# Optimization experiments

Measured on AMD Instinct MI355X. Metric: run time of the kernel, lower is better.

## Reference

```python
import jax, jax.numpy as jnp
import numpy as np

D_MODEL = 1024
H = 16
D_K = D_MODEL // H  # 64


def setup_inputs() -> dict:
    key = jax.random.key(0)
    ks = jax.random.split(key, 10)
    s = 1.0 / np.sqrt(D_MODEL)
    x = jax.random.normal(ks[0], (4, 2048, D_MODEL), dtype=jnp.float32)
    # Per-head linear weights stacked: [H, d_model, d_k]
    Wq = jax.random.uniform(ks[1], (H, D_MODEL, D_K), jnp.float32, -s, s)
    bq = jax.random.uniform(ks[2], (H, D_K), jnp.float32, -s, s)
    Wk = jax.random.uniform(ks[3], (H, D_MODEL, D_K), jnp.float32, -s, s)
    bk = jax.random.uniform(ks[4], (H, D_K), jnp.float32, -s, s)
    Wv = jax.random.uniform(ks[5], (H, D_MODEL, D_K), jnp.float32, -s, s)
    bv = jax.random.uniform(ks[6], (H, D_K), jnp.float32, -s, s)
    so = 1.0 / np.sqrt(H * D_K)
    Wo = jax.random.uniform(ks[7], (H * D_K, D_MODEL), jnp.float32, -so, so)
    bo = jax.random.uniform(ks[8], (D_MODEL,), jnp.float32, -so, so)
    return {"x": x, "Wq": Wq, "bq": bq, "Wk": Wk, "bk": bk, "Wv": Wv, "bv": bv, "Wo": Wo, "bo": bo}


def reference(x, Wq, bq, Wk, bk, Wv, bv, Wo, bo):
    # x: [B, S, D]; Wq/Wk/Wv: [H, D, d_k]; b*: [H, d_k]
    q = jnp.einsum('bsd,hdk->bhsk', x, Wq) + bq[None, :, None, :]
    k = jnp.einsum('bsd,hdk->bhsk', x, Wk) + bk[None, :, None, :]
    v = jnp.einsum('bsd,hdk->bhsk', x, Wv) + bv[None, :, None, :]
    scores = jnp.einsum('bhqk,bhsk->bhqs', q, k) / np.sqrt(D_K)
    S = x.shape[1]
    causal = jnp.triu(jnp.ones((S, S), dtype=bool), k=1)  # True above diagonal
    scores = jnp.where(causal, -jnp.inf, scores)
    attn = jax.nn.softmax(scores, axis=-1)
    ctx = jnp.einsum('bhqs,bhsk->bhqk', attn, v)  # [B, H, S, d_k]
    B = x.shape[0]
    # concat heads: torch cats head outputs along last dim -> [B, S, H*d_k]
    ctx = jnp.transpose(ctx, (0, 2, 1, 3)).reshape(B, S, H * D_K)
    return ctx @ Wo + bo
```

## Files before the change

kernel.cpp:

```cpp
#include <hip/hip_runtime.h>
#include <hip/hip_bf16.h>

typedef unsigned short u16;
typedef __attribute__((ext_vector_type(8))) short short8;
typedef __attribute__((ext_vector_type(4))) short short4v;
typedef __attribute__((ext_vector_type(4))) float floatx4;

#define D_MODEL 1024
#define NH 16
#define SEQ 2048
#define BATCH 4
#define M_ROWS 8192
#define N_QKV 3072
#define PS_LD 72

__device__ __forceinline__ u16 f2u(float f) {
    __hip_bfloat16 h = __float2bfloat16(f);
    u16 u; __builtin_memcpy(&u, &h, 2); return u;
}

__device__ __forceinline__ void async_copy16(const u16* g, u16* l) {
    __builtin_amdgcn_global_load_lds(
        (const __attribute__((address_space(1))) unsigned int*)(g),
        (__attribute__((address_space(3))) unsigned int*)(l),
        16, 0, 0);
}

__global__ __launch_bounds__(256) void prep(
    const float* __restrict__ x,
    const float* __restrict__ Wq, const float* __restrict__ Wk,
    const float* __restrict__ Wv, const float* __restrict__ Wo,
    const float* __restrict__ bq, const float* __restrict__ bk,
    const float* __restrict__ bv, const float* __restrict__ bo,
    u16* __restrict__ xb, u16* __restrict__ Wpt, u16* __restrict__ Wot,
    float* __restrict__ biasp)
{
    __shared__ u16 T[64 * 72];
    const int tid = threadIdx.x;
    const int blk = blockIdx.x;

    if (blk < 4096) {
        size_t i = ((size_t)blk * 256 + tid) * 8;
        float4 f0 = *(const float4*)&x[i];
        float4 f1 = *(const float4*)&x[i + 4];
        u16 t[8] = {f2u(f0.x), f2u(f0.y), f2u(f0.z), f2u(f0.w),
                    f2u(f1.x), f2u(f1.y), f2u(f1.z), f2u(f1.w)};
        *(short8*)&xb[i] = *(short8*)t;
        return;
    }
    if (blk == 5120) {
        #pragma unroll
        for (int j = 0; j < 16; j++) {
            int idx = j * 256 + tid;
            float v;
            if (idx < 1024)      v = bq[idx] * 0.125f;
            else if (idx < 2048) v = bk[idx - 1024];
            else if (idx < 3072) v = bv[idx - 2048];
            else                 v = bo[idx - 3072];
            biasp[idx] = v;
        }
        return;
    }
    const int wb = blk - 4096;
    const int r = tid >> 2, s4 = (tid & 3) * 16;
    if (wb < 768) {
        int sel = wb / 256, rem = wb % 256;
        int h = rem >> 4, ktile = rem & 15;
        const float* W = (sel == 0) ? Wq : ((sel == 1) ? Wk : Wv);
        const float scale = (sel == 0) ? 0.125f : 1.0f;
        const float* src = W + ((size_t)h * 1024 + ktile * 64 + r) * 64 + s4;
        #pragma unroll
        for (int i = 0; i < 16; i++) T[(s4 + i) * 72 + r] = f2u(src[i] * scale);
        __syncthreads();
        u16 tmp[16];
        #pragma unroll
        for (int i = 0; i < 16; i++) tmp[i] = T[r * 72 + s4 + i];
        u16* dst = Wpt + ((size_t)sel * 1024 + h * 64 + r) * 1024 + ktile * 64 + s4;
        *(short8*)&dst[0] = *(short8*)&tmp[0];
        *(short8*)&dst[8] = *(short8*)&tmp[8];
    } else {
        int rem = wb - 768;
        int nt = rem >> 4, kt2 = rem & 15;
        const float* src = Wo + ((size_t)kt2 * 64 + r) * 1024 + nt * 64 + s4;
        #pragma unroll
        for (int i = 0; i < 16; i++) T[(s4 + i) * 72 + r] = f2u(src[i]);
        __syncthreads();
        u16 tmp[16];
        #pragma unroll
        for (int i = 0; i < 16; i++) tmp[i] = T[r * 72 + s4 + i];
        u16* dst = Wot + ((size_t)nt * 64 + r) * 1024 + kt2 * 64 + s4;
        *(short8*)&dst[0] = *(short8*)&tmp[0];
        *(short8*)&dst[8] = *(short8*)&tmp[8];
    }
}

__global__ __launch_bounds__(256) void vtrans(const u16* __restrict__ QKV,
                                              u16* __restrict__ Vtg) {
    __shared__ u16 T[64 * 72];
    const int bh = blockIdx.x, kt = blockIdx.y;
    const int b = bh >> 4, h = bh & 15;
    const int tid = threadIdx.x;
    const int r = tid >> 2, s4 = (tid & 3) * 16;
    const u16* vp = QKV + (size_t)(b * SEQ + kt * 64 + r) * N_QKV + 2 * D_MODEL + h * 64 + s4;
    *(short8*)&T[r * 72 + s4]     = *(const short8*)&vp[0];
    *(short8*)&T[r * 72 + s4 + 8] = *(const short8*)&vp[8];
    __syncthreads();
    u16 tmp[16];
    #pragma unroll
    for (int i = 0; i < 16; i++) tmp[i] = T[(s4 + i) * 72 + r];
    u16* op = Vtg + ((size_t)bh * 64 + r) * SEQ + kt * 64 + s4;
    *(short8*)&op[0] = *(short8*)&tmp[0];
    *(short8*)&op[8] = *(short8*)&tmp[8];
}

template <typename OT>
__global__ __launch_bounds__(256) void gemm128(
    const u16* __restrict__ A, const u16* __restrict__ Bt,
    const float* __restrict__ bias, OT* __restrict__ C,
    int M, int N, int K)
{
    __shared__ u16 As[128 * 64];
    __shared__ u16 Bs[128 * 64];
    const int tid = threadIdx.x;
    const int w = tid >> 6, lane = tid & 63;
    const int l16 = lane & 15, quad = lane >> 4;
    const int bn = blockIdx.x * 128, bm = blockIdx.y * 128;
    const int wr = (w >> 1) * 64, wc = (w & 1) * 64;

    floatx4 acc[4][4];
    #pragma unroll
    for (int i = 0; i < 4; i++)
        #pragma unroll
        for (int j = 0; j < 4; j++) acc[i][j] = (floatx4){0.f, 0.f, 0.f, 0.f};

    for (int k0 = 0; k0 < K; k0 += 64) {
        #pragma unroll
        for (int c = 0; c < 4; c++) {
            const int off = (w * 4 + c) * 1024 + lane * 16;
            const int row = off >> 7, seg = (off >> 4) & 7;
            async_copy16(A  + (size_t)(bm + row) * K + k0 + seg * 8, &As[(w * 4 + c) * 512]);
            async_copy16(Bt + (size_t)(bn + row) * K + k0 + seg * 8, &Bs[(w * 4 + c) * 512]);
        }
        __syncthreads();
        #pragma unroll
        for (int kc = 0; kc < 2; kc++) {
            short8 a[4], b[4];
            #pragma unroll
            for (int i = 0; i < 4; i++)
                a[i] = *(short8*)&As[(wr + i * 16 + l16) * 64 + kc * 32 + quad * 8];
            #pragma unroll
            for (int i = 0; i < 4; i++)
                b[i] = *(short8*)&Bs[(wc + i * 16 + l16) * 64 + kc * 32 + quad * 8];
            #pragma unroll
            for (int mm = 0; mm < 4; mm++)
                #pragma unroll
                for (int nn = 0; nn < 4; nn++)
                    acc[mm][nn] = __builtin_amdgcn_mfma_f32_16x16x32_bf16(
                        a[mm], b[nn], acc[mm][nn], 0, 0, 0);
        }
        __syncthreads();
    }

    #pragma unroll
    for (int nn = 0; nn < 4; nn++) {
        const int col = bn + wc + nn * 16 + l16;
        const float bi = bias[col];
        #pragma unroll
        for (int mm = 0; mm < 4; mm++) {
            const int row = bm + wr + mm * 16 + quad * 4;
            #pragma unroll
            for (int r = 0; r < 4; r++) {
                float v = acc[mm][nn][r] + bi;
                if constexpr (sizeof(OT) == 2) ((u16*)C)[(size_t)(row + r) * N + col] = f2u(v);
                else                           C[(size_t)(row + r) * N + col] = v;
            }
        }
    }
}

#define G256_BAR   __builtin_amdgcn_s_barrier()
#define G256_LGKM0 { asm volatile("s_waitcnt lgkmcnt(0)" ::: "memory"); \
                     __builtin_amdgcn_sched_barrier(0); }

#define G256_STG(dstbase, s0, s1) { \
    async_copy16((s0), &lds[(dstbase) + stw]); \
    async_copy16((s1), &lds[(dstbase) + 4096 + stw]); }

#define G256_STAGE_A(bb, half, kq) \
    G256_STG((bb) * 32768 + (half) * 8192, \
             pA[0] + (size_t)(half) * hstep + (kq), \
             pA[1] + (size_t)(half) * hstep + (kq))

#define G256_STAGE_B(bb, half, kq) \
    G256_STG((bb) * 32768 + 16384 + (half) * 8192, \
             pB[0] + (size_t)(half) * hstep + (kq), \
             pB[1] + (size_t)(half) * hstep + (kq))

#define G256_LDA4(dst, bb, mi0) { \
    const int _b = (bb) * 32768 + wm * 8192; \
    _Pragma("unroll") \
    for (int mi = 0; mi < 4; mi++) { \
        const int _r = _b + (((mi0) + mi) * 16 + l16) * 64; \
        dst[mi * 2]     = *(const short8*)&lds[_r + col0]; \
        dst[mi * 2 + 1] = *(const short8*)&lds[_r + col1]; \
    } }

#define G256_LDB2(dst, bb, ni0) { \
    const int _b = (bb) * 32768 + 16384 + (wn >> 1) * 8192 + (wn & 1) * 4096; \
    _Pragma("unroll") \
    for (int ni = 0; ni < 2; ni++) { \
        const int _r = _b + (((ni0) + ni) * 16 + l16) * 64; \
        dst[ni * 2]     = *(const short8*)&lds[_r + col0]; \
        dst[ni * 2 + 1] = *(const short8*)&lds[_r + col1]; \
    } }

#define G256_MMA8(av, bv, MI0, NI0) { \
    _Pragma("unroll") \
    for (int mi = 0; mi < 4; mi++) \
    _Pragma("unroll") \
    for (int ni = 0; ni < 2; ni++) { \
        acc[(MI0) + mi][(NI0) + ni] = __builtin_amdgcn_mfma_f32_16x16x32_bf16( \
            av[mi * 2],     bv[ni * 2],     acc[(MI0) + mi][(NI0) + ni], 0, 0, 0); \
        acc[(MI0) + mi][(NI0) + ni] = __builtin_amdgcn_mfma_f32_16x16x32_bf16( \
            av[mi * 2 + 1], bv[ni * 2 + 1], acc[(MI0) + mi][(NI0) + ni], 0, 0, 0); \
    } }

template <typename OT>
__global__ __launch_bounds__(512, 2) void gemm256(
    const u16* __restrict__ A, const u16* __restrict__ Bt,
    const float* __restrict__ bias, OT* __restrict__ C,
    int M, int N, int K)
{
    __shared__ u16 lds[65536];
    const int tid = threadIdx.x;
    const int w = tid >> 6, lane = tid & 63;
    const int l16 = lane & 15, quad = lane >> 4;
    const int wm = w >> 2, wn = w & 3;
    const int bn = blockIdx.x * 256, bm = blockIdx.y * 256;

    const u16* pA[2]; const u16* pB[2];
    #pragma unroll
    for (int j = 0; j < 2; j++) {
        const int d = (j * 512 + tid) * 16;
        const int s = d ^ (((d >> 7) & 7) << 4);
        const int r = s >> 7;
        const int c = (s & 127) >> 1;
        pA[j] = A  + (size_t)(bm + r) * K + c;
        pB[j] = Bt + (size_t)(bn + r) * K + c;
    }
    const size_t hstep = (size_t)128 * K;
    const int stw = w * 512;

    const int xm = (l16 & 7) << 3;
    const int col0 = (quad * 8) ^ xm;
    const int col1 = (32 + quad * 8) ^ xm;

    floatx4 acc[8][4];
    #pragma unroll
    for (int i = 0; i < 8; i++)
        #pragma unroll
        for (int j = 0; j < 4; j++) acc[i][j] = (floatx4){0.f, 0.f, 0.f, 0.f};

    G256_STAGE_A(0, 0, 0);  G256_STAGE_A(0, 1, 0);
    G256_STAGE_B(0, 0, 0);  G256_STAGE_B(0, 1, 0);
    G256_STAGE_B(1, 0, 64); G256_STAGE_B(1, 1, 64);
    asm volatile("s_waitcnt vmcnt(0)" ::: "memory");
    __syncthreads();

    short8 aL[8], aH[8], bL[4], bH[4];
    const int NKT = K >> 6;
    for (int kt = 0; kt < NKT; ++kt) {
        const int buf = kt & 1, nb = buf ^ 1;
        const int kqA = (kt + 1) << 6, kqB = (kt + 2) << 6;
        const bool stA = (kt + 1 < NKT), stB = (kt + 2 < NKT);

        G256_LDA4(aL, buf, 0);
        G256_LDB2(bL, buf, 0);
        if (stA) { G256_STAGE_A(nb, 0, kqA); }
        asm volatile("s_waitcnt lgkmcnt(8)" ::: "memory");
        G256_BAR; G256_LGKM0;
        __builtin_amdgcn_s_setprio(1); G256_MMA8(aL, bL, 0, 0);
        __builtin_amdgcn_s_setprio(0); G256_BAR;

        G256_LDB2(bH, buf, 2);
        if (stA) { G256_STAGE_A(nb, 1, kqA); }
        G256_BAR; G256_LGKM0;
        __builtin_amdgcn_s_setprio(1); G256_MMA8(aL, bH, 0, 2);
        __builtin_amdgcn_s_setprio(0); G256_BAR;

        G256_LDA4(aH, buf, 4);
        if (stB) { G256_STAGE_B(buf, 0, kqB); }
        G256_BAR; G256_LGKM0;
        __builtin_amdgcn_s_setprio(1); G256_MMA8(aH, bH, 4, 2);
        __builtin_amdgcn_s_setprio(0); G256_BAR;

        if (stB) {
            G256_STAGE_B(buf, 1, kqB);
            asm volatile("s_waitcnt vmcnt(4)" ::: "memory");
        } else if (stA) {
            asm volatile("s_waitcnt vmcnt(0)" ::: "memory");
        }
        G256_BAR;
        __builtin_amdgcn_s_setprio(1); G256_MMA8(aH, bL, 4, 0);
        __builtin_amdgcn_s_setprio(0); G256_BAR;
    }

    #pragma unroll
    for (int ni = 0; ni < 4; ni++) {
        const int col = bn + wn * 64 + ni * 16 + l16;
        const float bi = bias[col];
        #pragma unroll
        for (int mi = 0; mi < 8; mi++) {
            const int row = bm + wm * 128 + mi * 16 + quad * 4;
            #pragma unroll
            for (int r = 0; r < 4; r++) {
                float v = acc[mi][ni][r] + bi;
                if constexpr (sizeof(OT) == 2) ((u16*)C)[(size_t)(row + r) * N + col] = f2u(v);
                else                           C[(size_t)(row + r) * N + col] = v;
            }
        }
    }
}

__global__ __launch_bounds__(256) void attn_mfma(
    const u16* __restrict__ QKV, const u16* __restrict__ Vtg, u16* __restrict__ ctx)
{
    __shared__ u16 Ks[2][64 * 64];
    __shared__ u16 Vs[2][64 * 64];
    __shared__ u16 Ps[128 * PS_LD];

    const int bh = blockIdx.x;
    const int qt = (int)(gridDim.y - 1) - (int)blockIdx.y;
    const int b = bh >> 4, h = bh & 15;
    const int tid = threadIdx.x;
    const int w = tid >> 6, lane = tid & 63;
    const int l16 = lane & 15, quad = lane >> 4;

    const int r0 = tid >> 3,        c0 = tid & 7;
    const int r1 = (256 + tid) >> 3, c1 = tid & 7;
    const int sw0 = c0 ^ (r0 & 7), sw1 = c1 ^ (r1 & 7);

    short8 q[2][2];
    #pragma unroll
    for (int m = 0; m < 2; m++) {
        const u16* qp = QKV + (size_t)(b * SEQ + qt * 128 + w * 32 + m * 16 + l16) * N_QKV + h * 64;
        q[m][0] = *(const short8*)&qp[quad * 8];
        q[m][1] = *(const short8*)&qp[32 + quad * 8];
    }

    floatx4 O[2][4];
    #pragma unroll
    for (int m = 0; m < 2; m++)
        #pragma unroll
        for (int i = 0; i < 4; i++) O[m][i] = (floatx4){0.f, 0.f, 0.f, 0.f};
    float li[2] = {0.f, 0.f};

    const int nkt = 2 * qt + 2;
    const int qrow_w_max = qt * 128 + w * 32 + 31;

    const size_t kbase = (size_t)(b * SEQ) * N_QKV + D_MODEL + h * 64;
    const size_t vbase = (size_t)bh * 64 * SEQ;

    {
        float4 ka = *(const float4*)(QKV + kbase + (size_t)(0 + r0) * N_QKV + c0 * 8);
        float4 kb = *(const float4*)(QKV + kbase + (size_t)(0 + r1) * N_QKV + c1 * 8);
        float4 va = *(const float4*)(Vtg + vbase + (size_t)r0 * SEQ + 0 + c0 * 8);
        float4 vb = *(const float4*)(Vtg + vbase + (size_t)r1 * SEQ + 0 + c1 * 8);
        *(float4*)&Ks[0][r0 * 64 + sw0 * 8] = ka;
        *(float4*)&Ks[0][r1 * 64 + sw1 * 8] = kb;
        *(float4*)&Vs[0][r0 * 64 + sw0 * 8] = va;
        *(float4*)&Vs[0][r1 * 64 + sw1 * 8] = vb;
    }
    __syncthreads();

    for (int kt = 0; kt < nkt; kt++) {
        const int buf = kt & 1;
        const bool pre = (kt + 1 < nkt);
        float4 ka, kb, va, vb;
        if (pre) {
            const int t1 = (kt + 1) * 64;
            ka = *(const float4*)(QKV + kbase + (size_t)(t1 + r0) * N_QKV + c0 * 8);
            kb = *(const float4*)(QKV + kbase + (size_t)(t1 + r1) * N_QKV + c1 * 8);
            va = *(const float4*)(Vtg + vbase + (size_t)r0 * SEQ + t1 + c0 * 8);
            vb = *(const float4*)(Vtg + vbase + (size_t)r1 * SEQ + t1 + c1 * 8);
        }

        if (kt * 64 <= qrow_w_max) {
            short8 kf[4][2];
            #pragma unroll
            for (int ns = 0; ns < 4; ns++) {
                const int rr = ns * 16 + l16, rs = rr & 7;
                kf[ns][0] = *(short8*)&Ks[buf][rr * 64 + (quad ^ rs) * 8];
                kf[ns][1] = *(short8*)&Ks[buf][rr * 64 + ((4 + quad) ^ rs) * 8];
            }
            const bool needMask = (kt * 64 + 63 > qt * 128 + w * 32);

            #pragma unroll
            for (int m = 0; m < 2; m++) {
                floatx4 z[4];
                #pragma unroll
                for (int ns = 0; ns < 4; ns++) {
                    floatx4 t = (floatx4){0.f, 0.f, 0.f, 0.f};
                    t = __builtin_amdgcn_mfma_f32_16x16x32_bf16(kf[ns][0], q[m][0], t, 0, 0, 0);
                    t = __builtin_amdgcn_mfma_f32_16x16x32_bf16(kf[ns][1], q[m][1], t, 0, 0, 0);
                    z[ns] = t;
                }
                const int qrow_g = qt * 128 + w * 32 + m * 16 + l16;
                const int prow = (w * 32 + m * 16 + l16) * PS_LD;
                float sum = 0.f;
                #pragma unroll
                for (int ns = 0; ns < 4; ns++) {
                    u16 pk[4];
                    #pragma unroll
                    for (int r = 0; r < 4; r++) {
                        float s = z[ns][r];
                        const int key = kt * 64 + ns * 16 + quad * 4 + r;
                        if (needMask && key > qrow_g) s = -INFINITY;
                        float p = __expf(s - 8.0f);
                        pk[r] = f2u(p);
                        sum += p;
                    }
                    *(short4v*)&Ps[prow + ns * 16 + quad * 4] = *(short4v*)pk;
                }
                sum += __shfl_xor(sum, 16);
                sum += __shfl_xor(sum, 32);
                li[m] += sum;
            }

            short8 vf[4][2];
            #pragma unroll
            for (int ds = 0; ds < 4; ds++) {
                const int rr = ds * 16 + l16, rs = rr & 7;
                vf[ds][0] = *(short8*)&Vs[buf][rr * 64 + (quad ^ rs) * 8];
                vf[ds][1] = *(short8*)&Vs[buf][rr * 64 + ((4 + quad) ^ rs) * 8];
            }
            #pragma unroll
            for (int m = 0; m < 2; m++) {
                const int prow = (w * 32 + m * 16 + l16) * PS_LD;
                short8 p0 = *(short8*)&Ps[prow + quad * 8];
                short8 p1 = *(short8*)&Ps[prow + 32 + quad * 8];
                #pragma unroll
                for (int ds = 0; ds < 4; ds++) {
                    O[m][ds] = __builtin_amdgcn_mfma_f32_16x16x32_bf16(vf[ds][0], p0, O[m][ds], 0, 0, 0);
                    O[m][ds] = __builtin_amdgcn_mfma_f32_16x16x32_bf16(vf[ds][1], p1, O[m][ds], 0, 0, 0);
                }
            }
        }

        if (pre) {
            const int nb = buf ^ 1;
            *(float4*)&Ks[nb][r0 * 64 + sw0 * 8] = ka;
            *(float4*)&Ks[nb][r1 * 64 + sw1 * 8] = kb;
            *(float4*)&Vs[nb][r0 * 64 + sw0 * 8] = va;
            *(float4*)&Vs[nb][r1 * 64 + sw1 * 8] = vb;
        }
        __syncthreads();
    }

    #pragma unroll
    for (int m = 0; m < 2; m++) {
        const float inv = 1.0f / li[m];
        const size_t base = (size_t)(b * SEQ + qt * 128 + w * 32 + m * 16 + l16) * D_MODEL + h * 64;
        #pragma unroll
        for (int ds = 0; ds < 4; ds++) {
            u16 o[4];
            #pragma unroll
            for (int r = 0; r < 4; r++) o[r] = f2u(O[m][ds][r] * inv);
            *(short4v*)&ctx[base + ds * 16 + quad * 4] = *(short4v*)o;
        }
    }
}

extern "C" void kernel_launch(void* const* d_in, const int* in_sizes, int n_in,
                              void* d_out, int out_size, void* d_ws, size_t ws_size,
                              hipStream_t stream) {
    const float* x  = (const float*)d_in[0];
    const float* Wq = (const float*)d_in[1];
    const float* bq = (const float*)d_in[2];
    const float* Wk = (const float*)d_in[3];
    const float* bk = (const float*)d_in[4];
    const float* Wv = (const float*)d_in[5];
    const float* bv = (const float*)d_in[6];
    const float* Wo = (const float*)d_in[7];
    const float* bo = (const float*)d_in[8];
    float* out = (float*)d_out;

    char* ws = (char*)d_ws;
    float* biasp = (float*)ws;
    u16*   Wpt   = (u16*)(ws + 0x10000);
    u16*   Wot   = (u16*)(ws + 0x620000);
    u16*   xb    = (u16*)(ws + 0x840000);
    u16*   Vtg   = xb;
    u16*   QKV   = (u16*)(ws + 0x1840000);
    u16*   ctx   = (u16*)(ws + 0x4840000);

    prep<<<5121, 256, 0, stream>>>(x, Wq, Wk, Wv, Wo, bq, bk, bv, bo,
                                   xb, Wpt, Wot, biasp);

    gemm256<u16><<<dim3(N_QKV / 256, M_ROWS / 256), 512, 0, stream>>>(
        xb, Wpt, biasp, QKV, M_ROWS, N_QKV, D_MODEL);

    vtrans<<<dim3(64, 32), 256, 0, stream>>>(QKV, Vtg);

    attn_mfma<<<dim3(BATCH * NH, SEQ / 128), 256, 0, stream>>>(QKV, Vtg, ctx);

    gemm128<float><<<dim3(D_MODEL / 128, M_ROWS / 128), 256, 0, stream>>>(
        ctx, Wot, biasp + N_QKV, out, M_ROWS, D_MODEL, D_MODEL);
}
```

Measured before the change: 286.2 us.

## Use exp2 softmax, MFMA row sums, vectorized GEMM epilogue and setprio

```diff
diff --git a/kernel.cpp b/kernel.cpp
--- a/kernel.cpp
+++ b/kernel.cpp
@@ -13,6 +13,9 @@
 #define M_ROWS 8192
 #define N_QKV 3072
 #define PS_LD 72
+
+#define QSCALE 0.18033688011112042f
+#define EXP2_OFF 11.541560327111707f
 
 __device__ __forceinline__ u16 f2u(float f) {
     __hip_bfloat16 h = __float2bfloat16(f);
@@ -53,7 +56,7 @@
         for (int j = 0; j < 16; j++) {
             int idx = j * 256 + tid;
             float v;
-            if (idx < 1024)      v = bq[idx] * 0.125f;
+            if (idx < 1024)      v = bq[idx] * QSCALE;
             else if (idx < 2048) v = bk[idx - 1024];
             else if (idx < 3072) v = bv[idx - 2048];
             else                 v = bo[idx - 3072];
@@ -67,7 +70,7 @@
         int sel = wb / 256, rem = wb % 256;
         int h = rem >> 4, ktile = rem & 15;
         const float* W = (sel == 0) ? Wq : ((sel == 1) ? Wk : Wv);
-        const float scale = (sel == 0) ? 0.125f : 1.0f;
+        const float scale = (sel == 0) ? QSCALE : 1.0f;
         const float* src = W + ((size_t)h * 1024 + ktile * 64 + r) * 64 + s4;
         #pragma unroll
         for (int i = 0; i < 16; i++) T[(s4 + i) * 72 + r] = f2u(src[i] * scale);
@@ -220,9 +223,9 @@
     _Pragma("unroll") \
     for (int ni = 0; ni < 2; ni++) { \
         acc[(MI0) + mi][(NI0) + ni] = __builtin_amdgcn_mfma_f32_16x16x32_bf16( \
-            av[mi * 2],     bv[ni * 2],     acc[(MI0) + mi][(NI0) + ni], 0, 0, 0); \
+            bv[ni * 2],     av[mi * 2],     acc[(MI0) + mi][(NI0) + ni], 0, 0, 0); \
         acc[(MI0) + mi][(NI0) + ni] = __builtin_amdgcn_mfma_f32_16x16x32_bf16( \
-            av[mi * 2 + 1], bv[ni * 2 + 1], acc[(MI0) + mi][(NI0) + ni], 0, 0, 0); \
+            bv[ni * 2 + 1], av[mi * 2 + 1], acc[(MI0) + mi][(NI0) + ni], 0, 0, 0); \
     } }
 
 template <typename OT>
@@ -307,16 +310,21 @@
 
     #pragma unroll
     for (int ni = 0; ni < 4; ni++) {
-        const int col = bn + wn * 64 + ni * 16 + l16;
-        const float bi = bias[col];
+        const int col = bn + wn * 64 + ni * 16 + quad * 4;
+        const float4 bi = *(const float4*)&bias[col];
         #pragma unroll
         for (int mi = 0; mi < 8; mi++) {
-            const int row = bm + wm * 128 + mi * 16 + quad * 4;
-            #pragma unroll
-            for (int r = 0; r < 4; r++) {
-                float v = acc[mi][ni][r] + bi;
-                if constexpr (sizeof(OT) == 2) ((u16*)C)[(size_t)(row + r) * N + col] = f2u(v);
-                else                           C[(size_t)(row + r) * N + col] = v;
+            const int row = bm + wm * 128 + mi * 16 + l16;
+            const float v0 = acc[mi][ni][0] + bi.x;
+            const float v1 = acc[mi][ni][1] + bi.y;
+            const float v2 = acc[mi][ni][2] + bi.z;
+            const float v3 = acc[mi][ni][3] + bi.w;
+            if constexpr (sizeof(OT) == 2) {
+                u16 o[4] = {f2u(v0), f2u(v1), f2u(v2), f2u(v3)};
+                *(short4v*)&((u16*)C)[(size_t)row * N + col] = *(short4v*)o;
+            } else {
+                float4 fv = {v0, v1, v2, v3};
+                *(float4*)&C[(size_t)row * N + col] = fv;
             }
         }
     }
@@ -348,12 +356,18 @@
         q[m][1] = *(const short8*)&qp[32 + quad * 8];
     }
 
+    short8 ones8;
+    #pragma unroll
+    for (int i = 0; i < 8; i++) ones8[i] = (short)0x3F80;
+
     floatx4 O[2][4];
-    #pragma unroll
-    for (int m = 0; m < 2; m++)
+    floatx4 lsum[2];
+    #pragma unroll
+    for (int m = 0; m < 2; m++) {
+        lsum[m] = (floatx4){0.f, 0.f, 0.f, 0.f};
         #pragma unroll
         for (int i = 0; i < 4; i++) O[m][i] = (floatx4){0.f, 0.f, 0.f, 0.f};
-    float li[2] = {0.f, 0.f};
+    }
 
     const int nkt = 2 * qt + 2;
     const int qrow_w_max = qt * 128 + w * 32 + 31;
@@ -361,16 +375,23 @@
     const size_t kbase = (size_t)(b * SEQ) * N_QKV + D_MODEL + h * 64;
     const size_t vbase = (size_t)bh * 64 * SEQ;
 
+    const u16* kpa = QKV + kbase + (size_t)r0 * N_QKV + c0 * 8;
+    const u16* kpb = QKV + kbase + (size_t)r1 * N_QKV + c1 * 8;
+    const u16* vpa = Vtg + vbase + (size_t)r0 * SEQ + c0 * 8;
+    const u16* vpb = Vtg + vbase + (size_t)r1 * SEQ + c1 * 8;
+
     {
-        float4 ka = *(const float4*)(QKV + kbase + (size_t)(0 + r0) * N_QKV + c0 * 8);
-        float4 kb = *(const float4*)(QKV + kbase + (size_t)(0 + r1) * N_QKV + c1 * 8);
-        float4 va = *(const float4*)(Vtg + vbase + (size_t)r0 * SEQ + 0 + c0 * 8);
-        float4 vb = *(const float4*)(Vtg + vbase + (size_t)r1 * SEQ + 0 + c1 * 8);
+        float4 ka = *(const float4*)kpa;
+        float4 kb = *(const float4*)kpb;
+        float4 va = *(const float4*)vpa;
+        float4 vb = *(const float4*)vpb;
         *(float4*)&Ks[0][r0 * 64 + sw0 * 8] = ka;
         *(float4*)&Ks[0][r1 * 64 + sw1 * 8] = kb;
         *(float4*)&Vs[0][r0 * 64 + sw0 * 8] = va;
         *(float4*)&Vs[0][r1 * 64 + sw1 * 8] = vb;
     }
+    kpa += (size_t)64 * N_QKV; kpb += (size_t)64 * N_QKV;
+    vpa += 64; vpb += 64;
     __syncthreads();
 
     for (int kt = 0; kt < nkt; kt++) {
@@ -378,11 +399,12 @@
         const bool pre = (kt + 1 < nkt);
         float4 ka, kb, va, vb;
         if (pre) {
-            const int t1 = (kt + 1) * 64;
-            ka = *(const float4*)(QKV + kbase + (size_t)(t1 + r0) * N_QKV + c0 * 8);
-            kb = *(const float4*)(QKV + kbase + (size_t)(t1 + r1) * N_QKV + c1 * 8);
-            va = *(const float4*)(Vtg + vbase + (size_t)r0 * SEQ + t1 + c0 * 8);
-            vb = *(const float4*)(Vtg + vbase + (size_t)r1 * SEQ + t1 + c1 * 8);
+            ka = *(const float4*)kpa;
+            kb = *(const float4*)kpb;
+            va = *(const float4*)vpa;
+            vb = *(const float4*)vpb;
+            kpa += (size_t)64 * N_QKV; kpb += (size_t)64 * N_QKV;
+            vpa += 64; vpb += 64;
         }
 
         if (kt * 64 <= qrow_w_max) {
@@ -398,6 +420,7 @@
             #pragma unroll
             for (int m = 0; m < 2; m++) {
                 floatx4 z[4];
+                __builtin_amdgcn_s_setprio(1);
                 #pragma unroll
                 for (int ns = 0; ns < 4; ns++) {
                     floatx4 t = (floatx4){0.f, 0.f, 0.f, 0.f};
@@ -405,9 +428,9 @@
                     t = __builtin_amdgcn_mfma_f32_16x16x32_bf16(kf[ns][1], q[m][1], t, 0, 0, 0);
                     z[ns] = t;
                 }
+                __builtin_amdgcn_s_setprio(0);
                 const int qrow_g = qt * 128 + w * 32 + m * 16 + l16;
                 const int prow = (w * 32 + m * 16 + l16) * PS_LD;
-                float sum = 0.f;
                 #pragma unroll
                 for (int ns = 0; ns < 4; ns++) {
                     u16 pk[4];
@@ -416,15 +439,11 @@
                         float s = z[ns][r];
                         const int key = kt * 64 + ns * 16 + quad * 4 + r;
                         if (needMask && key > qrow_g) s = -INFINITY;
-                        float p = __expf(s - 8.0f);
+                        float p = __builtin_amdgcn_exp2f(s - EXP2_OFF);
                         pk[r] = f2u(p);
-                        sum += p;
                     }
                     *(short4v*)&Ps[prow + ns * 16 + quad * 4] = *(short4v*)pk;
                 }
-                sum += __shfl_xor(sum, 16);
-                sum += __shfl_xor(sum, 32);
-                li[m] += sum;
             }
 
             short8 vf[4][2];
@@ -434,17 +453,21 @@
                 vf[ds][0] = *(short8*)&Vs[buf][rr * 64 + (quad ^ rs) * 8];
                 vf[ds][1] = *(short8*)&Vs[buf][rr * 64 + ((4 + quad) ^ rs) * 8];
             }
+            __builtin_amdgcn_s_setprio(1);
             #pragma unroll
             for (int m = 0; m < 2; m++) {
                 const int prow = (w * 32 + m * 16 + l16) * PS_LD;
                 short8 p0 = *(short8*)&Ps[prow + quad * 8];
                 short8 p1 = *(short8*)&Ps[prow + 32 + quad * 8];
+                lsum[m] = __builtin_amdgcn_mfma_f32_16x16x32_bf16(ones8, p0, lsum[m], 0, 0, 0);
+                lsum[m] = __builtin_amdgcn_mfma_f32_16x16x32_bf16(ones8, p1, lsum[m], 0, 0, 0);
                 #pragma unroll
                 for (int ds = 0; ds < 4; ds++) {
                     O[m][ds] = __builtin_amdgcn_mfma_f32_16x16x32_bf16(vf[ds][0], p0, O[m][ds], 0, 0, 0);
                     O[m][ds] = __builtin_amdgcn_mfma_f32_16x16x32_bf16(vf[ds][1], p1, O[m][ds], 0, 0, 0);
                 }
             }
+            __builtin_amdgcn_s_setprio(0);
         }
 
         if (pre) {
@@ -459,7 +482,7 @@
 
     #pragma unroll
     for (int m = 0; m < 2; m++) {
-        const float inv = 1.0f / li[m];
+        const float inv = 1.0f / lsum[m][0];
         const size_t base = (size_t)(b * SEQ + qt * 128 + w * 32 + m * 16 + l16) * D_MODEL + h * 64;
         #pragma unroll
         for (int ds = 0; ds < 4; ds++) {
```

After: 283.2 us. No clear change (-1.1%).
